# Kernel tuning notes

Measured on AMD Instinct MI355X. Metric: run time of the kernel, lower is better.

Reference implementation:

```python
import jax, jax.numpy as jnp
import numpy as np

DIM = 33  # hardcoded in the torch module


def setup_inputs() -> dict:
    key = jax.random.key(0)
    k1, k2, k3 = jax.random.split(key, 3)
    B, H, W = 8, 512, 512
    inp = jax.random.uniform(k1, (B, 3, H, W), dtype=jnp.float32)
    out = jax.random.uniform(k2, (B, 3, H, W), dtype=jnp.float32)
    mask = (jax.random.uniform(k3, (B, 1, H, W)) > 0.5).astype(jnp.float32)
    return {"mask": mask, "input": inp, "output": out}


def _tridistribute(mask, inp, out, dim=DIM):
    # Trilinear scatter-accumulate of `out` pixel colors into a per-image
    # 3D LUT indexed by `inp` pixel colors, masked, then count-normalized.
    B = inp.shape[0]
    binsize = 1.000001 / (dim - 1)
    x = inp / binsize                              # [B,3,H,W]
    idx = jnp.floor(x).astype(jnp.int32)           # lower bin ids, in [0, dim-2]
    frac = x - jnp.floor(x)                        # trilinear fractions
    r_id, g_id, b_id = idx[:, 0], idx[:, 1], idx[:, 2]
    rd = frac[:, 0].reshape(B, -1)                 # [B,N], N = H*W
    gd = frac[:, 1].reshape(B, -1)
    bd = frac[:, 2].reshape(B, -1)
    base = (r_id + g_id * dim + b_id * dim * dim).reshape(B, -1)  # flat corner 000
    m = (mask[:, 0] > 0).astype(inp.dtype).reshape(B, -1)
    ws, offs = [], []
    for db in (0, 1):
        for dg in (0, 1):
            for dr in (0, 1):
                w = ((rd if dr else 1 - rd) * (gd if dg else 1 - gd) * (bd if db else 1 - bd))
                ws.append(w * m)
                offs.append(dr + dg * dim + db * dim * dim)
    w_all = jnp.stack(ws, 0)                                        # [8,B,N]
    idx_all = base[None] + jnp.asarray(offs, jnp.int32)[:, None, None]  # [8,B,N]
    idx_flat = idx_all.transpose(1, 0, 2).reshape(B, -1)            # [B,8N]
    w_flat = w_all.transpose(1, 0, 2).reshape(B, -1)                # [B,8N]
    out_f = out.reshape(B, 3, -1)                                   # [B,3,N]
    vals = (w_all[:, :, None, :] * out_f[None]).transpose(1, 2, 0, 3).reshape(B, 3, -1)  # [B,3,8N]
    nbins = dim ** 3
    # scatter-add per batch element (vmap over B, then over 3 channels)
    lut = jax.vmap(lambda i, v: jax.vmap(lambda vc: jnp.zeros(nbins, inp.dtype).at[i].add(vc))(v))(idx_flat, vals)  # [B,3,nbins]
    cnt1 = jax.vmap(lambda i, w: jnp.zeros(nbins, inp.dtype).at[i].add(w))(idx_flat, w_flat)  # [B,nbins]
    cnt = jnp.broadcast_to(cnt1[:, None, :], lut.shape)             # same count for all 3 channels
    denom = jnp.where(cnt > 0, cnt, 1.0)
    lut = jnp.where(cnt > 0, lut / denom, 0.0)                      # tridistribute.divide
    shape5 = (B, 3, dim, dim, dim)
    return lut.reshape(shape5), cnt.reshape(shape5)


def reference(mask, input, output):
    lut, lut_count = _tridistribute(mask, input, output)
    return lut, lut_count, output
```

## Files before the change

kernel.cpp:

```cpp
#include <hip/hip_runtime.h>
#include <hip/hip_fp16.h>

#define DIM   33
#define NB    (DIM * DIM * DIM)
#define BATCH 8
#define HW    (512 * 512)
#define SLICE (DIM * DIM)
#define NK1   32
#define CAP1  4416
#define W1    256
#define SPAN1 1024
#define SUB2  4
#define NKEY  1024
#define CAP2  192
#define MAXC2 1120

#define G1_OFF 0
#define G2_OFF 256
#define NCNT   (G2_OFF + BATCH * NKEY)
#define A1     8448
#define S1     (BATCH * NK1 * CAP1)
#define A2     (A1 + 3 * S1)
#define S2     (BATCH * NKEY * CAP2)
#define WS_WORDS (A2 + 3 * S2)

#define WAVE_LDS_FENCE() do { \
    asm volatile("s_waitcnt lgkmcnt(0)" ::: "memory"); \
    __builtin_amdgcn_sched_barrier(0); \
} while (0)

static __device__ __forceinline__ unsigned f2h(float x) {
    return (unsigned)__half_as_ushort(__float2half(x));
}
static __device__ __forceinline__ float h2f(unsigned u) {
    return __half2float(__ushort_as_half((unsigned short)(u & 0xffffu)));
}
static __device__ __forceinline__ unsigned pack2(float a, float b) {
    return f2h(a) | (f2h(b) << 16);
}

__global__ __launch_bounds__(256) void zero_counters(int* __restrict__ ws)
{
    int i = blockIdx.x * 256 + threadIdx.x;
    if (i < NCNT) ws[i] = 0;
}

__global__ __launch_bounds__(256) void sort1(const float* __restrict__ mask,
                                             const float* __restrict__ inp,
                                             const float* __restrict__ outp,
                                             int* __restrict__ ws,
                                             float* __restrict__ outcopy)
{
    __shared__ int hist[NK1], basev[NK1], startL[NK1];
    __shared__ unsigned       stX[SPAN1];
    __shared__ unsigned       stY[SPAN1];
    __shared__ unsigned       o01[SPAN1];
    __shared__ unsigned short o2h[SPAN1];
    __shared__ unsigned short rnk[SPAN1];
    __shared__ unsigned short sidx[SPAN1];

    const int bid = blockIdx.x;
    const int w   = bid & (W1 - 1);
    const int b   = bid >> 8;

    if (threadIdx.x < NK1) hist[threadIdx.x] = 0;
    __syncthreads();

    const float binsize = 1.000001f / 32.0f;
    const size_t off = (size_t)w * SPAN1;
    const float* mk  = mask + (size_t)b * HW + off;
    const float* inR = inp  + (size_t)b * 3 * HW + off;
    const float* inG = inR + HW;
    const float* inB = inR + 2 * HW;
    const float* oR  = outp + (size_t)b * 3 * HW + off;
    const float* oG  = oR + HW;
    const float* oB  = oR + 2 * HW;
    float* cR = outcopy + (size_t)b * 3 * HW + off;
    float* cG = cR + HW;
    float* cB = cR + 2 * HW;

    const int o = threadIdx.x * 4;

    {
        float4 mv = *(const float4*)(mk + o);
        float4 rv = *(const float4*)(inR + o);
        float4 gv = *(const float4*)(inG + o);
        float4 bv = *(const float4*)(inB + o);
        float4 a0 = *(const float4*)(oR + o);
        float4 a1 = *(const float4*)(oG + o);
        float4 a2 = *(const float4*)(oB + o);

        *(float4*)(cR + o) = a0;
        *(float4*)(cG + o) = a1;
        *(float4*)(cB + o) = a2;

        float mm[4] = {mv.x, mv.y, mv.z, mv.w};
        float rr[4] = {rv.x, rv.y, rv.z, rv.w};
        float gg[4] = {gv.x, gv.y, gv.z, gv.w};
        float bb[4] = {bv.x, bv.y, bv.z, bv.w};
        float q0[4] = {a0.x, a0.y, a0.z, a0.w};
        float q1[4] = {a1.x, a1.y, a1.z, a1.w};
        float q2[4] = {a2.x, a2.y, a2.z, a2.w};
        #pragma unroll
        for (int r = 0; r < 4; ++r) {
            o01[o + r] = pack2(q0[r], q1[r]);
            o2h[o + r] = (unsigned short)f2h(q2[r]);
            unsigned sx = 0, sy = 0;
            if (mm[r] > 0.0f) {
                float xr = rr[r] / binsize;
                float xg = gg[r] / binsize;
                float xb = bb[r] / binsize;
                float fr = floorf(xr), fg = floorf(xg), fb = floorf(xb);
                int ir = (int)fr, ig = (int)fg, ib = (int)fb;
                int rd12 = (int)((xr - fr) * 4095.0f + 0.5f);
                int gd12 = (int)((xg - fg) * 4095.0f + 0.5f);
                int bd12 = (int)((xb - fb) * 4095.0f + 0.5f);
                sx = (unsigned)ir | ((unsigned)ig << 5) | ((unsigned)rd12 << 10)
                   | ((unsigned)(gd12 & 0x3FF) << 22);
                sy = (unsigned)(gd12 >> 10) | ((unsigned)bd12 << 2)
                   | ((unsigned)ib << 14) | (1u << 19);
                rnk[o + r] = (unsigned short)atomicAdd(&hist[ib], 1);
            }
            stX[o + r] = sx;
            stY[o + r] = sy;
        }
    }
    __syncthreads();

    if (threadIdx.x < NK1) {
        int c = hist[threadIdx.x];
        basev[threadIdx.x] = c ? atomicAdd(&ws[G1_OFF + b * NK1 + threadIdx.x], c) : 0;
        int v = c;
        #pragma unroll
        for (int d = 1; d < 32; d <<= 1) {
            int t = __shfl_up(v, d);
            if (threadIdx.x >= d) v += t;
        }
        startL[threadIdx.x] = v - c;
    }
    __syncthreads();

    {
        #pragma unroll
        for (int r = 0; r < 4; ++r) {
            unsigned sy = stY[o + r];
            if (sy >> 19) {
                int k = (sy >> 14) & 31;
                sidx[startL[k] + rnk[o + r]] = (unsigned short)(o + r);
            }
        }
    }
    __syncthreads();

    const int nlive = startL[NK1 - 1] + hist[NK1 - 1];
    unsigned* x1 = (unsigned*)(ws + A1);
    unsigned* y1 = x1 + S1;
    unsigned* z1 = x1 + 2 * S1;
    for (int j = threadIdx.x; j < nlive; j += 256) {
        int t = sidx[j];
        unsigned sy = stY[t];
        int k = (sy >> 14) & 31;
        int gs = basev[k] + (j - startL[k]);
        if (gs < CAP1) {
            size_t base = (size_t)(b * NK1 + k) * CAP1 + gs;
            x1[base] = stX[t];
            y1[base] = (sy & 0x3FFFu) | ((o01[t] & 0xFFFFu) << 14);
            z1[base] = (o01[t] >> 16) | ((unsigned)o2h[t] << 16);
        }
    }
}

__global__ __launch_bounds__(256) void sort2(int* __restrict__ ws)
{
    __shared__ unsigned       xL[MAXC2], yL[MAXC2], zL[MAXC2];
    __shared__ unsigned short rnkL[MAXC2], sidxL[MAXC2];
    __shared__ int hist[32], basev[32], startL[32];

    const int bid = blockIdx.x;
    const int s   = bid & (SUB2 - 1);
    const int ib  = (bid >> 2) & 31;
    const int b   = bid >> 7;

    if (threadIdx.x < 32) hist[threadIdx.x] = 0;
    __syncthreads();

    int n1 = ws[G1_OFF + b * NK1 + ib];
    if (n1 > CAP1) n1 = CAP1;
    const int beg = n1 * s / SUB2;
    const int end = n1 * (s + 1) / SUB2;
    const int cntn = end - beg;

    const unsigned* x1 = (const unsigned*)(ws + A1);
    const unsigned* y1 = x1 + S1;
    const unsigned* z1 = x1 + 2 * S1;
    const size_t base1 = (size_t)(b * NK1 + ib) * CAP1 + beg;

    for (int i = threadIdx.x; i < cntn; i += 256) {
        unsigned x = x1[base1 + i];
        xL[i] = x;
        yL[i] = y1[base1 + i];
        zL[i] = z1[base1 + i];
        rnkL[i] = (unsigned short)atomicAdd(&hist[(x >> 5) & 31], 1);
    }
    __syncthreads();

    if (threadIdx.x < 32) {
        int c = hist[threadIdx.x];
        basev[threadIdx.x] = c
            ? atomicAdd(&ws[G2_OFF + ((b << 10) | (threadIdx.x << 5) | ib)], c) : 0;
        int v = c;
        #pragma unroll
        for (int d = 1; d < 32; d <<= 1) {
            int t = __shfl_up(v, d);
            if (threadIdx.x >= d) v += t;
        }
        startL[threadIdx.x] = v - c;
    }
    __syncthreads();

    for (int i = threadIdx.x; i < cntn; i += 256) {
        int k = (xL[i] >> 5) & 31;
        sidxL[startL[k] + rnkL[i]] = (unsigned short)i;
    }
    __syncthreads();

    unsigned* x2 = (unsigned*)(ws + A2);
    unsigned* y2 = x2 + S2;
    unsigned* z2 = x2 + 2 * S2;
    for (int j = threadIdx.x; j < cntn; j += 256) {
        int t = sidxL[j];
        unsigned x = xL[t];
        int k = (x >> 5) & 31;
        int gs = basev[k] + (j - startL[k]);
        if (gs < CAP2) {
            size_t b2 = (size_t)((b << 10) | (k << 5) | ib) * CAP2 + gs;
            x2[b2] = x;
            y2[b2] = yL[t];
            z2[b2] = zL[t];
        }
    }
}

__global__ __launch_bounds__(256) void gather_pass(const int* __restrict__ ws,
                                                   float* __restrict__ lut,
                                                   float* __restrict__ cnt)
{
    __shared__ float4 vL[4][CAP2];
    __shared__ float  rdL[4][CAP2];
    __shared__ int    histL[4][32];
    __shared__ int    startL[4][32];
    __shared__ float  partL[4][64][4];

    const int bid   = blockIdx.x;
    const int b     = bid / SLICE;
    const int rem   = bid % SLICE;
    const int gOut  = rem / DIM;
    const int blOut = rem % DIM;

    const int wv    = threadIdx.x >> 6;
    const int lane  = threadIdx.x & 63;
    const int ghalf = (wv >> 1) & 1;
    const int bhalf = wv & 1;
    const int ig    = gOut - 1 + ghalf;
    const int ib    = blOut - 1 + bhalf;
    const bool valid = ((unsigned)ig < 32u) && ((unsigned)ib < 32u);

    if (lane < 32) histL[wv][lane] = 0;

    const unsigned* x2 = (const unsigned*)(ws + A2);
    const unsigned* y2 = x2 + S2;
    const unsigned* z2 = x2 + 2 * S2;

    unsigned rx[3] = {0, 0, 0}, ry[3] = {0, 0, 0}, rz[3] = {0, 0, 0};
    int n = 0;
    if (valid) {
        int key = (b << 10) | ((ig << 5) | ib);
        size_t kb = (size_t)key * CAP2;
        #pragma unroll
        for (int t = 0; t < 3; ++t) {
            int i = lane + t * 64;
            rx[t] = x2[kb + i];
            ry[t] = y2[kb + i];
            rz[t] = z2[kb + i];
        }
        n = ws[G2_OFF + key];
        if (n > CAP2) n = CAP2;
    }
    WAVE_LDS_FENCE();

    const float inv = 1.0f / 4095.0f;
    int    ranks[3] = {0, 0, 0};
    int    irs[3]   = {0, 0, 0};
    float4 vreg[3];
    float  rdreg[3] = {0.f, 0.f, 0.f};
    if (valid) {
        #pragma unroll
        for (int t = 0; t < 3; ++t) {
            unsigned x = rx[t], y = ry[t], z = rz[t];
            float rd = (float)((x >> 10) & 0xFFF) * inv;
            float gd = (float)(((x >> 22) & 0x3FF) | ((y & 3u) << 10)) * inv;
            float bd = (float)((y >> 2) & 0xFFF) * inv;
            float o0 = h2f(y >> 14);
            float o1 = h2f(z);
            float o2 = h2f(z >> 16);
            float wg_ = ghalf ? (1.0f - gd) : gd;
            float wb_ = bhalf ? (1.0f - bd) : bd;
            float wgb = wg_ * wb_;
            vreg[t]  = make_float4(wgb * o0, wgb * o1, wgb * o2, wgb);
            rdreg[t] = rd;
            irs[t]   = x & 31;
            int i = lane + t * 64;
            if (i < n) ranks[t] = atomicAdd(&histL[wv][irs[t]], 1);
        }
    }
    WAVE_LDS_FENCE();

    {
        int h = (lane < 32) ? histL[wv][lane] : 0;
        int v = h;
        #pragma unroll
        for (int o = 1; o < 32; o <<= 1) {
            int t = __shfl_up(v, o, 32);
            if ((lane & 31) >= o) v += t;
        }
        if (lane < 32) startL[wv][lane] = v - h;
    }
    WAVE_LDS_FENCE();

    if (valid) {
        #pragma unroll
        for (int t = 0; t < 3; ++t) {
            int i = lane + t * 64;
            if (i < n) {
                int pos = startL[wv][irs[t]] + ranks[t];
                vL[wv][pos]  = vreg[t];
                rdL[wv][pos] = rdreg[t];
            }
        }
    }
    WAVE_LDS_FENCE();

    float4 acc = make_float4(0.f, 0.f, 0.f, 0.f);
    if (valid) {
        const int run = lane >> 1;
        const int kk  = lane & 1;
        int s = startL[wv][run];
        int e = s + histL[wv][run];
        for (int j = s; j < e; ++j) {
            float4 v = vL[wv][j];
            float rd = rdL[wv][j];
            float wr_ = kk ? (1.0f - rd) : rd;
            acc.x += wr_ * v.x;
            acc.y += wr_ * v.y;
            acc.z += wr_ * v.z;
            acc.w += wr_ * v.w;
        }
    }
    *(float4*)partL[wv][lane] = acc;
    __syncthreads();

    if (threadIdx.x < DIM * 4) {
        int r  = threadIdx.x >> 2;
        int ch = threadIdx.x & 3;
        float v = 0.f, c = 0.f;
        #pragma unroll
        for (int w2 = 0; w2 < 4; ++w2) {
            if (r < 32) {
                v += partL[w2][2 * r + 1][ch == 3 ? 3 : ch];
                c += partL[w2][2 * r + 1][3];
            }
            if (r > 0) {
                v += partL[w2][2 * r - 2][ch == 3 ? 3 : ch];
                c += partL[w2][2 * r - 2][3];
            }
        }
        int bin = r + gOut * DIM + blOut * SLICE;
        size_t ob = (size_t)b * 3 * NB;
        if (ch == 3) {
            cnt[ob + bin]          = c;
            cnt[ob + NB + bin]     = c;
            cnt[ob + 2 * NB + bin] = c;
        } else {
            lut[ob + (size_t)ch * NB + bin] = (c > 0.0f) ? v / c : 0.0f;
        }
    }
}

__global__ void tridist_scatter(const float* __restrict__ mask,
                                const float* __restrict__ inp,
                                const float* __restrict__ outp,
                                float* __restrict__ lut,
                                float* __restrict__ cnt)
{
    int i = blockIdx.x * blockDim.x + threadIdx.x;
    if (i >= BATCH * HW) return;
    int b = i / HW;
    int p = i - b * HW;

    float m = mask[(size_t)b * HW + p];
    if (!(m > 0.0f)) return;

    const float binsize = 1.000001f / 32.0f;
    size_t ibase = (size_t)b * 3 * HW + p;
    float xr = inp[ibase] / binsize;
    float xg = inp[ibase + HW] / binsize;
    float xb = inp[ibase + 2 * HW] / binsize;
    float flr = floorf(xr), flg = floorf(xg), flb = floorf(xb);
    int ir = (int)flr, ig = (int)flg, ib = (int)flb;
    float rd = xr - flr, gd = xg - flg, bd = xb - flb;
    int base = ir + ig * DIM + ib * DIM * DIM;
    float o0 = outp[ibase], o1 = outp[ibase + HW], o2 = outp[ibase + 2 * HW];
    float wr[2] = {1.0f - rd, rd};
    float wg_[2] = {1.0f - gd, gd};
    float wb[2] = {1.0f - bd, bd};
    float* lut0 = lut + (size_t)b * 3 * NB;
    float* cnt0 = cnt + (size_t)b * 3 * NB;
    #pragma unroll
    for (int db = 0; db < 2; ++db)
        #pragma unroll
        for (int dg = 0; dg < 2; ++dg)
            #pragma unroll
            for (int dr = 0; dr < 2; ++dr) {
                float wv2 = (wr[dr] * wg_[dg]) * wb[db];
                int bin = base + dr + dg * DIM + db * DIM * DIM;
                atomicAdd(cnt0 + bin, wv2);
                atomicAdd(lut0 + bin, wv2 * o0);
                atomicAdd(lut0 + NB + bin, wv2 * o1);
                atomicAdd(lut0 + 2 * NB + bin, wv2 * o2);
            }
}

__global__ void tridist_finalize(float* __restrict__ lut, float* __restrict__ cnt)
{
    int i = blockIdx.x * blockDim.x + threadIdx.x;
    if (i >= BATCH * NB) return;
    int b = i / NB;
    int j = i - b * NB;
    float c = cnt[(size_t)b * 3 * NB + j];
    bool nz = (c > 0.0f);
    #pragma unroll
    for (int ch = 0; ch < 3; ++ch) {
        size_t off = ((size_t)b * 3 + ch) * NB + j;
        float v = lut[off];
        lut[off] = nz ? (v / c) : 0.0f;
        cnt[off] = c;
    }
}

__global__ void copy_out(const float4* __restrict__ src,
                         float4* __restrict__ dst, int n4)
{
    int i = blockIdx.x * blockDim.x + threadIdx.x;
    int stride = gridDim.x * blockDim.x;
    for (; i < n4; i += stride) dst[i] = src[i];
}

extern "C" void kernel_launch(void* const* d_in, const int* in_sizes, int n_in,
                              void* d_out, int out_size, void* d_ws, size_t ws_size,
                              hipStream_t stream)
{
    const float* mask = (const float*)d_in[0];
    const float* inp  = (const float*)d_in[1];
    const float* outp = (const float*)d_in[2];

    float* out     = (float*)d_out;
    float* lut     = out;
    float* cnt     = out + (size_t)BATCH * 3 * NB;
    float* outcopy = out + (size_t)2 * BATCH * 3 * NB;

    size_t need = (size_t)WS_WORDS * sizeof(int);

    if (ws_size >= need) {
        int* ws = (int*)d_ws;
        zero_counters<<<(NCNT + 255) / 256, 256, 0, stream>>>(ws);
        sort1<<<BATCH * W1, 256, 0, stream>>>(mask, inp, outp, ws, outcopy);
        sort2<<<BATCH * NK1 * SUB2, 256, 0, stream>>>(ws);
        gather_pass<<<BATCH * SLICE, 256, 0, stream>>>(ws, lut, cnt);
    } else {
        hipMemsetAsync(out, 0, (size_t)2 * BATCH * 3 * NB * sizeof(float), stream);
        tridist_scatter<<<(BATCH * HW + 255) / 256, 256, 0, stream>>>(mask, inp, outp, lut, cnt);
        tridist_finalize<<<(BATCH * NB + 255) / 256, 256, 0, stream>>>(lut, cnt);
        int n4 = BATCH * 3 * HW / 4;
        copy_out<<<2048, 256, 0, stream>>>((const float4*)outp, (float4*)outcopy, n4);
    }
}
```

Before: 60.42 us.

## Give each wave a full output row in gather_pass and reduce via shuffles

gather_pass now maps each wavefront to one complete (gOut, blOut) output row and processes all four neighbouring source keys itself, so a block covers four rows and the grid shrinks by four. The cross-wave partial-sum LDS buffer and the block-wide __syncthreads are replaced by wave shuffles that combine the adjacent-r partials. Staged weighted colours and weights are packed as half pairs in LDS to cut shared-memory traffic. In exchange, register and LDS use per block rise, which may lower occupancy, and fp16 staging of the weighted values reduces precision before fp32 accumulation.

```diff
diff --git a/kernel.cpp b/kernel.cpp
--- a/kernel.cpp
+++ b/kernel.cpp
@@ -14,6 +14,7 @@
 #define NKEY  1024
 #define CAP2  192
 #define MAXC2 1120
+#define GROWS (BATCH * SLICE)
 
 #define G1_OFF 0
 #define G2_OFF 256
@@ -245,143 +246,163 @@
                                                    float* __restrict__ lut,
                                                    float* __restrict__ cnt)
 {
-    __shared__ float4 vL[4][CAP2];
-    __shared__ float  rdL[4][CAP2];
-    __shared__ int    histL[4][32];
-    __shared__ int    startL[4][32];
-    __shared__ float  partL[4][64][4];
-
-    const int bid   = blockIdx.x;
-    const int b     = bid / SLICE;
-    const int rem   = bid % SLICE;
+    __shared__ unsigned pA[4][4][CAP2];
+    __shared__ unsigned pB[4][4][CAP2];
+    __shared__ float    pR[4][4][CAP2];
+    __shared__ int      histL[4][4][32];
+    __shared__ int      startL[4][4][32];
+
+    const int wv   = threadIdx.x >> 6;
+    const int lane = threadIdx.x & 63;
+    const int row  = blockIdx.x * 4 + wv;
+    const int b     = row / SLICE;
+    const int rem   = row % SLICE;
     const int gOut  = rem / DIM;
     const int blOut = rem % DIM;
 
-    const int wv    = threadIdx.x >> 6;
-    const int lane  = threadIdx.x & 63;
-    const int ghalf = (wv >> 1) & 1;
-    const int bhalf = wv & 1;
-    const int ig    = gOut - 1 + ghalf;
-    const int ib    = blOut - 1 + bhalf;
-    const bool valid = ((unsigned)ig < 32u) && ((unsigned)ib < 32u);
-
-    if (lane < 32) histL[wv][lane] = 0;
+    if (lane < 32) {
+        #pragma unroll
+        for (int q = 0; q < 4; ++q) histL[wv][q][lane] = 0;
+    }
 
     const unsigned* x2 = (const unsigned*)(ws + A2);
     const unsigned* y2 = x2 + S2;
     const unsigned* z2 = x2 + 2 * S2;
 
-    unsigned rx[3] = {0, 0, 0}, ry[3] = {0, 0, 0}, rz[3] = {0, 0, 0};
-    int n = 0;
-    if (valid) {
-        int key = (b << 10) | ((ig << 5) | ib);
-        size_t kb = (size_t)key * CAP2;
-        #pragma unroll
-        for (int t = 0; t < 3; ++t) {
-            int i = lane + t * 64;
-            rx[t] = x2[kb + i];
-            ry[t] = y2[kb + i];
-            rz[t] = z2[kb + i];
-        }
-        n = ws[G2_OFF + key];
-        if (n > CAP2) n = CAP2;
-    }
+    int      nq[4];
+    size_t   kb[4];
+    bool     vq[4];
+    unsigned rx[4][3], ry[4][3], rz[4][3];
+    #pragma unroll
+    for (int q = 0; q < 4; ++q) {
+        int ig = gOut - 1 + (q >> 1);
+        int ib = blOut - 1 + (q & 1);
+        vq[q] = ((unsigned)ig < 32u) && ((unsigned)ib < 32u);
+        nq[q] = 0;
+        if (vq[q]) {
+            int key = (b << 10) | (ig << 5) | ib;
+            kb[q] = (size_t)key * CAP2;
+            nq[q] = ws[G2_OFF + key];
+            #pragma unroll
+            for (int t = 0; t < 3; ++t) {
+                int i = lane + t * 64;
+                rx[q][t] = x2[kb[q] + i];
+                ry[q][t] = y2[kb[q] + i];
+                rz[q][t] = z2[kb[q] + i];
+            }
+        }
+    }
+    #pragma unroll
+    for (int q = 0; q < 4; ++q) if (nq[q] > CAP2) nq[q] = CAP2;
     WAVE_LDS_FENCE();
 
     const float inv = 1.0f / 4095.0f;
-    int    ranks[3] = {0, 0, 0};
-    int    irs[3]   = {0, 0, 0};
-    float4 vreg[3];
-    float  rdreg[3] = {0.f, 0.f, 0.f};
-    if (valid) {
-        #pragma unroll
-        for (int t = 0; t < 3; ++t) {
-            unsigned x = rx[t], y = ry[t], z = rz[t];
-            float rd = (float)((x >> 10) & 0xFFF) * inv;
-            float gd = (float)(((x >> 22) & 0x3FF) | ((y & 3u) << 10)) * inv;
-            float bd = (float)((y >> 2) & 0xFFF) * inv;
-            float o0 = h2f(y >> 14);
-            float o1 = h2f(z);
-            float o2 = h2f(z >> 16);
-            float wg_ = ghalf ? (1.0f - gd) : gd;
-            float wb_ = bhalf ? (1.0f - bd) : bd;
-            float wgb = wg_ * wb_;
-            vreg[t]  = make_float4(wgb * o0, wgb * o1, wgb * o2, wgb);
-            rdreg[t] = rd;
-            irs[t]   = x & 31;
-            int i = lane + t * 64;
-            if (i < n) ranks[t] = atomicAdd(&histL[wv][irs[t]], 1);
+    unsigned wA[4][3], wB[4][3];
+    float    rdv[4][3];
+    int      irx[4][3], rk[4][3];
+    #pragma unroll
+    for (int q = 0; q < 4; ++q) {
+        const int ghalf = q >> 1, bhalf = q & 1;
+        if (vq[q]) {
+            #pragma unroll
+            for (int t = 0; t < 3; ++t) {
+                unsigned x = rx[q][t], y = ry[q][t], z = rz[q][t];
+                float rd = (float)((x >> 10) & 0xFFF) * inv;
+                float gd = (float)(((x >> 22) & 0x3FF) | ((y & 3u) << 10)) * inv;
+                float bd = (float)((y >> 2) & 0xFFF) * inv;
+                float o0 = h2f(y >> 14);
+                float o1 = h2f(z);
+                float o2 = h2f(z >> 16);
+                float wg_ = ghalf ? (1.0f - gd) : gd;
+                float wb_ = bhalf ? (1.0f - bd) : bd;
+                float wgb = wg_ * wb_;
+                wA[q][t]  = pack2(wgb * o0, wgb * o1);
+                wB[q][t]  = pack2(wgb * o2, wgb);
+                rdv[q][t] = rd;
+                irx[q][t] = x & 31;
+                int i = lane + t * 64;
+                rk[q][t] = (i < nq[q]) ? atomicAdd(&histL[wv][q][irx[q][t]], 1) : 0;
+            }
         }
     }
     WAVE_LDS_FENCE();
 
-    {
-        int h = (lane < 32) ? histL[wv][lane] : 0;
+    #pragma unroll
+    for (int q = 0; q < 4; ++q) {
+        int h = (lane < 32) ? histL[wv][q][lane] : 0;
         int v = h;
         #pragma unroll
         for (int o = 1; o < 32; o <<= 1) {
             int t = __shfl_up(v, o, 32);
             if ((lane & 31) >= o) v += t;
         }
-        if (lane < 32) startL[wv][lane] = v - h;
+        if (lane < 32) startL[wv][q][lane] = v - h;
     }
     WAVE_LDS_FENCE();
 
-    if (valid) {
-        #pragma unroll
-        for (int t = 0; t < 3; ++t) {
-            int i = lane + t * 64;
-            if (i < n) {
-                int pos = startL[wv][irs[t]] + ranks[t];
-                vL[wv][pos]  = vreg[t];
-                rdL[wv][pos] = rdreg[t];
+    #pragma unroll
+    for (int q = 0; q < 4; ++q) {
+        if (vq[q]) {
+            #pragma unroll
+            for (int t = 0; t < 3; ++t) {
+                int i = lane + t * 64;
+                if (i < nq[q]) {
+                    int pos = startL[wv][q][irx[q][t]] + rk[q][t];
+                    pA[wv][q][pos] = wA[q][t];
+                    pB[wv][q][pos] = wB[q][t];
+                    pR[wv][q][pos] = rdv[q][t];
+                }
             }
         }
     }
     WAVE_LDS_FENCE();
 
-    float4 acc = make_float4(0.f, 0.f, 0.f, 0.f);
-    if (valid) {
+    float a0 = 0.f, a1 = 0.f, a2 = 0.f, a3 = 0.f;
+    {
         const int run = lane >> 1;
         const int kk  = lane & 1;
-        int s = startL[wv][run];
-        int e = s + histL[wv][run];
-        for (int j = s; j < e; ++j) {
-            float4 v = vL[wv][j];
-            float rd = rdL[wv][j];
-            float wr_ = kk ? (1.0f - rd) : rd;
-            acc.x += wr_ * v.x;
-            acc.y += wr_ * v.y;
-            acc.z += wr_ * v.z;
-            acc.w += wr_ * v.w;
-        }
-    }
-    *(float4*)partL[wv][lane] = acc;
-    __syncthreads();
-
-    if (threadIdx.x < DIM * 4) {
-        int r  = threadIdx.x >> 2;
-        int ch = threadIdx.x & 3;
-        float v = 0.f, c = 0.f;
-        #pragma unroll
-        for (int w2 = 0; w2 < 4; ++w2) {
-            if (r < 32) {
-                v += partL[w2][2 * r + 1][ch == 3 ? 3 : ch];
-                c += partL[w2][2 * r + 1][3];
-            }
-            if (r > 0) {
-                v += partL[w2][2 * r - 2][ch == 3 ? 3 : ch];
-                c += partL[w2][2 * r - 2][3];
-            }
-        }
-        int bin = r + gOut * DIM + blOut * SLICE;
-        size_t ob = (size_t)b * 3 * NB;
-        if (ch == 3) {
-            cnt[ob + bin]          = c;
-            cnt[ob + NB + bin]     = c;
-            cnt[ob + 2 * NB + bin] = c;
-        } else {
-            lut[ob + (size_t)ch * NB + bin] = (c > 0.0f) ? v / c : 0.0f;
+        #pragma unroll
+        for (int q = 0; q < 4; ++q) {
+            int s = startL[wv][q][run];
+            int e = s + histL[wv][q][run];
+            for (int j = s; j < e; ++j) {
+                unsigned aw = pA[wv][q][j];
+                unsigned bw = pB[wv][q][j];
+                float rd = pR[wv][q][j];
+                float wr_ = kk ? (1.0f - rd) : rd;
+                a0 += wr_ * h2f(aw);
+                a1 += wr_ * h2f(aw >> 16);
+                a2 += wr_ * h2f(bw);
+                a3 += wr_ * h2f(bw >> 16);
+            }
+        }
+    }
+
+    {
+        int r  = lane;
+        int s1 = (2 * r + 1) & 63;
+        int s2 = (2 * r - 2) & 63;
+        float v0 = __shfl(a0, s1) , u0 = __shfl(a0, s2);
+        float v1 = __shfl(a1, s1) , u1 = __shfl(a1, s2);
+        float v2 = __shfl(a2, s1) , u2 = __shfl(a2, s2);
+        float v3 = __shfl(a3, s1) , u3 = __shfl(a3, s2);
+        bool hi = (r < 32);
+        bool lo = (r > 0);
+        float res0 = (hi ? v0 : 0.f) + (lo ? u0 : 0.f);
+        float res1 = (hi ? v1 : 0.f) + (lo ? u1 : 0.f);
+        float res2 = (hi ? v2 : 0.f) + (lo ? u2 : 0.f);
+        float res3 = (hi ? v3 : 0.f) + (lo ? u3 : 0.f);
+
+        if (r < DIM) {
+            int bin = r + gOut * DIM + blOut * SLICE;
+            size_t ob = (size_t)b * 3 * NB;
+            bool nz = res3 > 0.0f;
+            lut[ob + bin]          = nz ? res0 / res3 : 0.0f;
+            lut[ob + NB + bin]     = nz ? res1 / res3 : 0.0f;
+            lut[ob + 2 * NB + bin] = nz ? res2 / res3 : 0.0f;
+            cnt[ob + bin]          = res3;
+            cnt[ob + NB + bin]     = res3;
+            cnt[ob + 2 * NB + bin] = res3;
         }
     }
 }
@@ -475,7 +496,7 @@
         zero_counters<<<(NCNT + 255) / 256, 256, 0, stream>>>(ws);
         sort1<<<BATCH * W1, 256, 0, stream>>>(mask, inp, outp, ws, outcopy);
         sort2<<<BATCH * NK1 * SUB2, 256, 0, stream>>>(ws);
-        gather_pass<<<BATCH * SLICE, 256, 0, stream>>>(ws, lut, cnt);
+        gather_pass<<<GROWS / 4, 256, 0, stream>>>(ws, lut, cnt);
     } else {
         hipMemsetAsync(out, 0, (size_t)2 * BATCH * 3 * NB * sizeof(float), stream);
         tridist_scatter<<<(BATCH * HW + 255) / 256, 256, 0, stream>>>(mask, inp, outp, lut, cnt);
```

After: 62.79 us. 3.9% more time.
